# Kernel tuning notes

Hardware: AMD Instinct MI355X
Metric: run time of the kernel (lower is better)

The kernel has to match this reference:

```python
import jax, jax.numpy as jnp
import numpy as np

EPS = 1e-5
B, S, D = 4, 2048, 128
BALL_SCALE = 0.05  # keeps points inside the unit Poincare ball for c=1


def setup_inputs() -> dict:
    key = jax.random.key(0)
    kq, kk, kv = jax.random.split(key, 3)
    q = jax.random.normal(kq, (B, S, D), dtype=jnp.float32) * BALL_SCALE
    k = jax.random.normal(kk, (B, S, D), dtype=jnp.float32) * BALL_SCALE
    v_tangent = jax.random.normal(kv, (B, S, D), dtype=jnp.float32)
    c = jnp.asarray(1.0, dtype=jnp.float32)
    beta = jnp.asarray(0.0, dtype=jnp.float32)            # nn.Parameter init 0.0
    attention_bias = jnp.asarray(0.0, dtype=jnp.float32)  # nn.Parameter init 0.0
    return {"q": q, "k": k, "v_tangent": v_tangent, "c": c,
            "beta": beta, "attention_bias": attention_bias}


def reference(q, k, v_tangent, c, beta, attention_bias):
    sqrt_c = jnp.sqrt(c)

    # --- pairwise Poincare distance (all fp32, as in the torch autocast block) ---
    x_norm_sq = jnp.sum(q * q, axis=-1, keepdims=True)            # (B,S,1)
    y_norm_sq = jnp.sum(k * k, axis=-1, keepdims=True)            # (B,S,1)
    xy_dot = jnp.einsum('bsd,btd->bst', q, k)                     # (B,S,S)
    y_norm_sq_t = jnp.swapaxes(y_norm_sq, -2, -1)                 # (B,1,S)
    diff_norm_sq = x_norm_sq - 2.0 * xy_dot + y_norm_sq_t         # ||x-y||^2, (B,S,S)
    denom = (1.0 - c * x_norm_sq) * (1.0 - c * y_norm_sq_t)       # (B,S,S)
    arg = 1.0 + 2.0 * c * diff_norm_sq / jnp.maximum(denom, EPS)
    dist = jnp.arccosh(jnp.maximum(arg, 1.0 + EPS)) / sqrt_c      # (B,S,S)

    # --- attention ---
    beta_positive = jax.nn.softplus(beta)
    attention_scores = -beta_positive * dist - attention_bias
    attention_weights = jax.nn.softmax(attention_scores, axis=-1)  # (B,S,S)
    output_tangent = jnp.einsum('bst,btd->bsd', attention_weights, v_tangent)

    # --- exp map at origin ---
    v_norm = jnp.maximum(
        jnp.sqrt(jnp.sum(output_tangent * output_tangent, axis=-1, keepdims=True)), EPS)
    output_hyperbolic = (jnp.tanh(sqrt_c * v_norm) / sqrt_c) * (output_tangent / v_norm)

    return output_hyperbolic, attention_weights
```

## Files before the change

kernel.cpp:

```cpp
#include <hip/hip_runtime.h>
#include <math.h>

#define B_ 4
#define S_ 2048
#define D_ 128
#define EPSF 1e-5f
#define BN 128
#define PSB 272

typedef __attribute__((ext_vector_type(8))) short short8;
typedef __attribute__((ext_vector_type(4))) float f32x4;

static __device__ __forceinline__ unsigned short f2bf(float f) {
    unsigned u = __float_as_uint(f);
    return (unsigned short)((u + 0x7fffu + ((u >> 16) & 1u)) >> 16);
}

static __device__ __forceinline__ void gload_lds16(const void* g, void* l) {
    __builtin_amdgcn_global_load_lds((const __attribute__((address_space(1))) unsigned*)g,
                                     (__attribute__((address_space(3))) unsigned*)l, 16, 0, 0);
}


__global__ __launch_bounds__(256) void convqk_kernel(const float* __restrict__ q,
                                                     const float* __restrict__ k,
                                                     const float* __restrict__ cp,
                                                     float* __restrict__ qn, float* __restrict__ kn,
                                                     float* __restrict__ lws,
                                                     float2* __restrict__ qng, float2* __restrict__ kng,
                                                     unsigned* __restrict__ Qb, unsigned* __restrict__ Kb) {
    int row = blockIdx.x * 4 + (threadIdx.x >> 6);
    int lane = threadIdx.x & 63;
    const int NR = B_ * S_;
    const float cc = cp[0];
    bool isQ = row < NR;
    int r = isQ ? row : row - NR;
    float2 v = ((const float2*)(isQ ? q : k))[(size_t)r * 64 + lane];
    unsigned pk = (unsigned)f2bf(v.x) | ((unsigned)f2bf(v.y) << 16);
    float nrm = v.x * v.x + v.y * v.y;
#pragma unroll
    for (int m = 1; m <= 32; m <<= 1) nrm += __shfl_xor(nrm, m, 64);
    if (isQ) {
        Qb[(size_t)r * 64 + lane] = pk;
        if (lane == 0) {
            qn[r] = nrm;
            qng[r] = make_float2(nrm, 2.f * cc * __builtin_amdgcn_rcpf(1.f - cc * nrm));
        }
        if (lane == 1) lws[r] = 0.f;
    } else {
        int c = lane >> 2;
        int cs = c ^ (r & 7);
        Kb[(size_t)r * 64 + cs * 4 + (lane & 3)] = pk;
        if (lane == 0) {
            kn[r] = nrm;
            kng[r] = make_float2(nrm, __builtin_amdgcn_rcpf(1.f - cc * nrm));
        }
    }
}

__global__ __launch_bounds__(256) void convv_kernel(const float* __restrict__ v, uint4* __restrict__ Vtb) {
    __shared__ unsigned short Vs[128 * 132];
    int b = blockIdx.x >> 4;
    int t = blockIdx.x & 15;
    int tid = threadIdx.x;
    const float* src = v + ((size_t)b * S_ + t * 128) * D_;
    int d4 = tid & 31, key0 = tid >> 5;
#pragma unroll
    for (int it = 0; it < 16; ++it) {
        int key = key0 + it * 8;
        float4 f = *(const float4*)(src + (size_t)key * D_ + d4 * 4);
        unsigned short* dst = &Vs[key * 132 + d4 * 4];
        dst[0] = f2bf(f.x); dst[1] = f2bf(f.y); dst[2] = f2bf(f.z); dst[3] = f2bf(f.w);
    }
    __syncthreads();
    uint4* tile = Vtb + (size_t)blockIdx.x * (128 * 16);
    int d = tid & 127;
    int cl = tid >> 7;
#pragma unroll
    for (int it = 0; it < 8; ++it) {
        int c = cl + it * 2;
        int kb = c * 8;
        unsigned short e0 = Vs[(kb + 0) * 132 + d], e1 = Vs[(kb + 1) * 132 + d];
        unsigned short e2 = Vs[(kb + 2) * 132 + d], e3 = Vs[(kb + 3) * 132 + d];
        unsigned short e4 = Vs[(kb + 4) * 132 + d], e5 = Vs[(kb + 5) * 132 + d];
        unsigned short e6 = Vs[(kb + 6) * 132 + d], e7 = Vs[(kb + 7) * 132 + d];
        uint4 o;
        o.x = (unsigned)e0 | ((unsigned)e1 << 16);
        o.y = (unsigned)e2 | ((unsigned)e3 << 16);
        o.z = (unsigned)e4 | ((unsigned)e5 << 16);
        o.w = (unsigned)e6 | ((unsigned)e7 << 16);
        tile[d * 16 + (c ^ (d & 7))] = o;
    }
}


__global__ __launch_bounds__(1024, 4) void hattn5_kernel(
    const unsigned short* __restrict__ Qb, const char* __restrict__ Kb, const char* __restrict__ Vtb,
    const float2* __restrict__ qng, const float2* __restrict__ kng,
    const float* __restrict__ cp, const float* __restrict__ betap, const float* __restrict__ biasp,
    uint4* __restrict__ Pws, float* __restrict__ hout, float* __restrict__ wout) {

    __shared__ __align__(1024) char smem[142336];
    char* PsB = smem + 131072;
    float* l_row = (float*)(smem + 142080);
    float* nsq_s = (float*)(smem + 142208);

    const int tid = threadIdx.x;
    const int lane = tid & 63, wave = tid >> 6;
    const int wm = wave & 1, wn = wave >> 1;
    const int lm = lane & 15, quad = lane >> 4;

    int xcd = blockIdx.x & 7;
    int b = xcd >> 1;
    int rb = (blockIdx.x >> 3) * 2 + (xcd & 1);
    int s0 = rb * 32;
    const size_t bS = (size_t)b * S_;

    const float beta = betap[0], bias = biasp[0];
    const float cc = cp[0];
    const float beta_pos = fmaxf(beta, 0.f) + log1pf(__expf(-fabsf(beta)));
    const float sqrt_c = sqrtf(cc);
    const float bneg = -beta_pos / sqrt_c;
    const float bias2 = -bias * 1.442695040888963f;
    const float onepe = 1.f + EPSF;

    const char* KbBase = Kb + bS * 256;
    const char* VtBase = Vtb + (size_t)b * 16 * 32768;

    {
#pragma unroll
        for (int j = 0; j < 2; ++j) {
            int m = tid + j * 1024;
            gload_lds16(KbBase + m * 16, smem + m * 16);
            gload_lds16(VtBase + m * 16, smem + 65536 + m * 16);
        }
        if (tid < 128) {
            float2 y = kng[bS + tid];
            *(float2*)(smem + 139776 + tid * 8) = y;
        } else if (tid < 160) {
            float2 x = qng[bS + s0 + (tid - 128)];
            *(float2*)(smem + 141824 + (tid - 128) * 8) = x;
        } else if (tid < 192) {
            l_row[tid - 160] = 0.f;
        } else if (tid < 224) {
            nsq_s[tid - 192] = 0.f;
        }
    }

    short8 aq[4];
    {
        const unsigned short* qrow = Qb + (bS + s0 + wm * 16 + lm) * D_;
#pragma unroll
        for (int ks = 0; ks < 4; ++ks)
            aq[ks] = *(const short8*)(qrow + ks * 32 + quad * 8);
    }

    f32x4 o = {0.f, 0.f, 0.f, 0.f};
    float lacc[4] = {0.f, 0.f, 0.f, 0.f};

    __syncthreads();

    int p = 0;
    const int n0 = wn * 16 + lm;
    for (int it = 0; it < 16; ++it) {
        char* KsC = smem + p * 32768;
        char* VtC = smem + 65536 + p * 32768;
        const char* YGC = smem + 139776 + p * 1024;

        float2 ygn;
        if (it < 15) {
            const char* ks = KbBase + (size_t)(it + 1) * 32768;
            const char* vs = VtBase + (size_t)(it + 1) * 32768;
            char* kd = smem + (p ^ 1) * 32768;
            char* vd = smem + 65536 + (p ^ 1) * 32768;
#pragma unroll
            for (int j = 0; j < 2; ++j) {
                int off = (tid + j * 1024) * 16;
                gload_lds16(ks + off, kd + off);
                gload_lds16(vs + off, vd + off);
            }
            if (tid < 128) ygn = kng[bS + (size_t)(it + 1) * 128 + tid];
        }

        f32x4 acc = {0.f, 0.f, 0.f, 0.f};
#pragma unroll
        for (int ks = 0; ks < 4; ++ks) {
            int c = ks * 4 + quad;
            short8 bk = *(const short8*)(KsC + n0 * 256 + ((c ^ (n0 & 7)) * 16));
            acc = __builtin_amdgcn_mfma_f32_16x16x32_bf16(aq[ks], bk, acc, 0, 0, 0);
        }

        {
            float2 yg = *(const float2*)(YGC + n0 * 8);
#pragma unroll
            for (int r = 0; r < 4; ++r) {
                int row = wm * 16 + quad * 4 + r;
                float2 xr = *(const float2*)(smem + 141824 + row * 8);
                float diff = fmaf(-2.f, acc[r], xr.x + yg.x);
                float arg = fmaf(diff * yg.y, xr.y, 1.f);
                arg = fmaxf(arg, onepe);
                float w = arg + sqrtf(fmaf(arg, arg, -1.f));
                float pv = __builtin_amdgcn_exp2f(fmaf(bneg, __builtin_amdgcn_logf(w), bias2));
                *(unsigned short*)(PsB + row * PSB + n0 * 2) = f2bf(pv);
                lacc[r] += pv;
            }
        }
        __syncthreads();

        if (it < 15 && tid < 128) *(float2*)(smem + 139776 + (p ^ 1) * 1024 + tid * 8) = ygn;

        if (tid < 512) {
            int row = tid >> 4, ch = tid & 15;
            uint4 pv = *(const uint4*)(PsB + row * PSB + ch * 16);
            Pws[(((bS + s0 + row) * S_ + (size_t)it * 128) >> 3) + ch] = pv;
        }

#pragma unroll
        for (int ks = 0; ks < 4; ++ks) {
            short8 ap = *(const short8*)(PsB + (wm * 16 + lm) * PSB + (ks * 32 + quad * 8) * 2);
            int c = ks * 4 + quad;
            short8 vv = *(const short8*)(VtC + n0 * 256 + ((c ^ (n0 & 7)) * 16));
            o = __builtin_amdgcn_mfma_f32_16x16x32_bf16(ap, vv, o, 0, 0, 0);
        }
        __syncthreads();
        p ^= 1;
    }

#pragma unroll
    for (int r = 0; r < 4; ++r) {
        float s = lacc[r];
#pragma unroll
        for (int m = 1; m <= 8; m <<= 1) s += __shfl_xor(s, m, 64);
        if (lm == 0) atomicAdd(&l_row[wm * 16 + quad * 4 + r], s);
    }
    __syncthreads();

    float linv[4];
#pragma unroll
    for (int r = 0; r < 4; ++r) linv[r] = 1.f / l_row[wm * 16 + quad * 4 + r];

#pragma unroll
    for (int r = 0; r < 4; ++r) {
        float x = o[r] * linv[r];
        o[r] = x;
        float np = x * x;
#pragma unroll
        for (int m = 1; m <= 8; m <<= 1) np += __shfl_xor(np, m, 64);
        if (lm == 0) atomicAdd(&nsq_s[wm * 16 + quad * 4 + r], np);
    }
    __syncthreads();
#pragma unroll
    for (int r = 0; r < 4; ++r) {
        int row = wm * 16 + quad * 4 + r;
        float vn = fmaxf(sqrtf(nsq_s[row]), EPSF);
        float a = sqrt_c * vn;
        float th = 1.f - 2.f / (__expf(2.f * a) + 1.f);
        float sc = th / a;
        hout[(bS + s0 + row) * D_ + n0] = o[r] * sc;
    }

    {
        const uint4* psrc = Pws + (((bS + s0) * (size_t)S_) >> 3);
        float4* wdst = (float4*)(wout + (bS + s0) * (size_t)S_);
#pragma unroll
        for (int j = 0; j < 8; ++j) {
            int idx = tid + j * 1024;
            int row = idx >> 8;
            float lr = 1.f / l_row[row];
            uint4 u = psrc[idx];
            float4 f0, f1;
            f0.x = __uint_as_float(u.x << 16) * lr;
            f0.y = __uint_as_float(u.x & 0xffff0000u) * lr;
            f0.z = __uint_as_float(u.y << 16) * lr;
            f0.w = __uint_as_float(u.y & 0xffff0000u) * lr;
            f1.x = __uint_as_float(u.z << 16) * lr;
            f1.y = __uint_as_float(u.z & 0xffff0000u) * lr;
            f1.z = __uint_as_float(u.w << 16) * lr;
            f1.w = __uint_as_float(u.w & 0xffff0000u) * lr;
            wdst[idx * 2] = f0;
            wdst[idx * 2 + 1] = f1;
        }
    }
}


__global__ __launch_bounds__(512, 2) void hattn_kernel(
    const unsigned short* __restrict__ Qb, const char* __restrict__ Kb, const char* __restrict__ Vtb,
    const float* __restrict__ qn, const float* __restrict__ kn,
    const float* __restrict__ cp, const float* __restrict__ betap, const float* __restrict__ biasp,
    float* __restrict__ lws, float* __restrict__ houtg, float* __restrict__ woutg) {

    __shared__ __align__(1024) char smem[75136];
    char* KsB = smem;
    char* VtB = smem + 32768;
    char* PsB = smem + 65536;
    float* kn_s  = (float*)(smem + 74240);
    float* qn_s  = (float*)(smem + 74752);
    float* l_row = (float*)(smem + 74880);
    float* nsq_s = (float*)(smem + 75008);

    const int tid = threadIdx.x;
    const int lane = tid & 63, wave = tid >> 6;
    const int wm = wave & 1, wn = wave >> 1;
    const int lm = lane & 15, quad = lane >> 4;

    int xcd = blockIdx.x & 7;
    int b = xcd >> 1;
    int rb = (blockIdx.x >> 3) * 2 + (xcd & 1);
    int s0 = rb * 32;
    const size_t bS = (size_t)b * S_;

    const float cc = cp[0], beta = betap[0], bias = biasp[0];
    const float beta_pos = fmaxf(beta, 0.f) + log1pf(__expf(-fabsf(beta)));
    const float sqrt_c = sqrtf(cc);
    const float inv_sqrt_c = 1.f / sqrt_c;

    if (tid < 32) {
        qn_s[tid] = qn[bS + s0 + tid];
        l_row[tid] = 0.f;
        nsq_s[tid] = 0.f;
    }

    short8 aq[4];
    {
        const unsigned short* qrow = Qb + (bS + s0 + wm * 16 + lm) * D_;
#pragma unroll
        for (int ks = 0; ks < 4; ++ks)
            aq[ks] = *(const short8*)(qrow + ks * 32 + quad * 8);
    }

    f32x4 o0 = {0.f, 0.f, 0.f, 0.f}, o1 = {0.f, 0.f, 0.f, 0.f};

    const char* KbBase = Kb + bS * 256;
    const char* VtBase = Vtb + (size_t)b * 16 * 32768;

    for (int t = 0; t < S_ / BN; ++t) {
        int t0 = t * BN;
        __syncthreads();
        {
            const uint4* ksrc = (const uint4*)(KbBase + (size_t)t0 * 256);
            const uint4* vsrc = (const uint4*)(VtBase + (size_t)t * 32768);
            uint4* kd = (uint4*)KsB;
            uint4* vd = (uint4*)VtB;
#pragma unroll
            for (int i = 0; i < 4; ++i) {
                kd[tid + i * 512] = ksrc[tid + i * 512];
                vd[tid + i * 512] = vsrc[tid + i * 512];
            }
            if (tid < BN) kn_s[tid] = kn[bS + t0 + tid];
        }
        __syncthreads();

        f32x4 acc0 = {0.f, 0.f, 0.f, 0.f}, acc1 = {0.f, 0.f, 0.f, 0.f};
#pragma unroll
        for (int ks = 0; ks < 4; ++ks) {
            int n0 = wn * 32 + lm;
            int c = ks * 4 + quad;
            short8 b0 = *(const short8*)(KsB + n0 * 256 + ((c ^ (n0 & 7)) * 16));
            int n1 = n0 + 16;
            short8 b1 = *(const short8*)(KsB + n1 * 256 + ((c ^ (n1 & 7)) * 16));
            acc0 = __builtin_amdgcn_mfma_f32_16x16x32_bf16(aq[ks], b0, acc0, 0, 0, 0);
            acc1 = __builtin_amdgcn_mfma_f32_16x16x32_bf16(aq[ks], b1, acc1, 0, 0, 0);
        }

        float lp[4];
#pragma unroll
        for (int r = 0; r < 4; ++r) {
            int row = wm * 16 + quad * 4 + r;
            float xn = qn_s[row];
            float fx = 1.f - cc * xn;
            float p0, p1;
#pragma unroll
            for (int nt = 0; nt < 2; ++nt) {
                int col = wn * 32 + nt * 16 + lm;
                float dot = (nt == 0) ? acc0[r] : acc1[r];
                float yn = kn_s[col];
                float diff = xn - 2.f * dot + yn;
                float den = fmaxf(fx * (1.f - cc * yn), EPSF);
                float arg = fmaf(2.f * cc * diff, __builtin_amdgcn_rcpf(den), 1.f);
                arg = fmaxf(arg, 1.f + EPSF);
                float dist = __logf(arg + sqrtf(arg * arg - 1.f)) * inv_sqrt_c;
                float p = __expf(fmaf(-beta_pos, dist, -bias));
                woutg[(bS + s0 + row) * S_ + t0 + col] = p;
                *(unsigned short*)(PsB + row * PSB + col * 2) = f2bf(p);
                if (nt == 0) p0 = p; else p1 = p;
            }
            lp[r] = p0 + p1;
        }
#pragma unroll
        for (int r = 0; r < 4; ++r) {
            float s = lp[r];
#pragma unroll
            for (int m = 1; m <= 8; m <<= 1) s += __shfl_xor(s, m, 64);
            if (lm == 0) atomicAdd(&l_row[wm * 16 + quad * 4 + r], s);
        }
        __syncthreads();

#pragma unroll
        for (int ks = 0; ks < 4; ++ks) {
            short8 ap = *(const short8*)(PsB + (wm * 16 + lm) * PSB + (ks * 32 + quad * 8) * 2);
            int d0 = wn * 32 + lm;
            int c = ks * 4 + quad;
            short8 v0 = *(const short8*)(VtB + d0 * 256 + ((c ^ (d0 & 7)) * 16));
            int d1 = d0 + 16;
            short8 v1 = *(const short8*)(VtB + d1 * 256 + ((c ^ (d1 & 7)) * 16));
            o0 = __builtin_amdgcn_mfma_f32_16x16x32_bf16(ap, v0, o0, 0, 0, 0);
            o1 = __builtin_amdgcn_mfma_f32_16x16x32_bf16(ap, v1, o1, 0, 0, 0);
        }
    }
    __syncthreads();

    float xs0[4], xs1[4];
#pragma unroll
    for (int r = 0; r < 4; ++r) {
        int row = wm * 16 + quad * 4 + r;
        float linv = __builtin_amdgcn_rcpf(l_row[row]);
        float x0 = o0[r] * linv, x1 = o1[r] * linv;
        xs0[r] = x0; xs1[r] = x1;
        float np = x0 * x0 + x1 * x1;
#pragma unroll
        for (int m = 1; m <= 8; m <<= 1) np += __shfl_xor(np, m, 64);
        if (lm == 0) atomicAdd(&nsq_s[row], np);
    }
    if (tid < 32) lws[bS + s0 + tid] = l_row[tid];
    __syncthreads();
#pragma unroll
    for (int r = 0; r < 4; ++r) {
        int row = wm * 16 + quad * 4 + r;
        float vn = fmaxf(sqrtf(nsq_s[row]), EPSF);
        float a = sqrt_c * vn;
        float th = 1.f - 2.f * __builtin_amdgcn_rcpf(__expf(2.f * a) + 1.f);
        float sc = th / a;
        houtg[(bS + s0 + row) * D_ + wn * 32 + lm] = xs0[r] * sc;
        houtg[(bS + s0 + row) * D_ + wn * 32 + 16 + lm] = xs1[r] * sc;
    }
}

__global__ __launch_bounds__(256) void wnorm_kernel(float* __restrict__ w,
                                                    const float* __restrict__ lws) {
    size_t idx = (size_t)blockIdx.x * 256 + threadIdx.x;
    int row = (int)(idx >> 9);
    float linv = 1.f / lws[row];
    float4* p = (float4*)w + idx;
    float4 v = *p;
    v.x *= linv; v.y *= linv; v.z *= linv; v.w *= linv;
    *p = v;
}


extern "C" void kernel_launch(void* const* d_in, const int* in_sizes, int n_in,
                              void* d_out, int out_size, void* d_ws, size_t ws_size,
                              hipStream_t stream) {
    const float* q    = (const float*)d_in[0];
    const float* k    = (const float*)d_in[1];
    const float* v    = (const float*)d_in[2];
    const float* c    = (const float*)d_in[3];
    const float* beta = (const float*)d_in[4];
    const float* ab   = (const float*)d_in[5];

    float* out  = (float*)d_out;
    float* hout = out;
    float* wout = out + (size_t)B_ * S_ * D_;

    float* qn  = (float*)d_ws;
    float* kn  = qn + B_ * S_;
    float* lws = kn + B_ * S_;
    char*  wsb = (char*)d_ws;
    const size_t QG_OFF = 98304;
    const size_t KG_OFF = QG_OFF + 65536;
    const size_t QB_OFF = KG_OFF + 65536;
    const size_t KB_OFF = QB_OFF + 2097152;
    const size_t VT_OFF = KB_OFF + 2097152;
    const size_t NEED1  = VT_OFF + 2097152;
    const size_t PW_OFF = NEED1;
    const size_t NEED2  = PW_OFF + (size_t)B_ * S_ * S_ * 2;

    float2*  qng = (float2*)(wsb + QG_OFF);
    float2*  kng = (float2*)(wsb + KG_OFF);
    unsigned* Qb = (unsigned*)(wsb + QB_OFF);
    unsigned* Kb = (unsigned*)(wsb + KB_OFF);
    uint4*   Vtb = (uint4*)(wsb + VT_OFF);

    if (ws_size >= NEED2) {
        uint4* Pws = (uint4*)(wsb + PW_OFF);
        convqk_kernel<<<4096, 256, 0, stream>>>(q, k, c, qn, kn, lws, qng, kng, Qb, Kb);
        convv_kernel<<<64, 256, 0, stream>>>(v, Vtb);
        hattn5_kernel<<<256, 1024, 0, stream>>>((const unsigned short*)Qb, (const char*)Kb,
                                                (const char*)Vtb, qng, kng, c, beta, ab,
                                                Pws, hout, wout);
    } else {
        convqk_kernel<<<4096, 256, 0, stream>>>(q, k, c, qn, kn, lws, qng, kng, Qb, Kb);
        convv_kernel<<<64, 256, 0, stream>>>(v, Vtb);
        hattn_kernel<<<256, 512, 0, stream>>>((const unsigned short*)Qb, (const char*)Kb,
                                              (const char*)Vtb, qn, kn, c, beta, ab,
                                              lws, hout, wout);
        wnorm_kernel<<<(B_ * S_ * S_ / 4) / 256, 256, 0, stream>>>(wout, lws);
    }
}
```

Baseline: 147.6 us.

## Keep full probability row block in LDS and stream K/V fragments into registers

The attention kernel now keeps the whole 32x2048 bf16 probability block in shared memory instead of spilling each 128-column tile to a global workspace and reading it back for normalization. K and V tiles are no longer staged through LDS with async global-to-LDS copies. Each wave loads its own K and V fragments straight from global memory into registers, prefetching the next K tile one step ahead. This removes a global round trip of the probability matrix and one barrier per iteration, but it loses the shared LDS reuse of K/V across waves and exposes global load latency.

```diff
diff --git a/kernel.cpp b/kernel.cpp
--- a/kernel.cpp
+++ b/kernel.cpp
@@ -7,6 +7,7 @@
 #define EPSF 1e-5f
 #define BN 128
 #define PSB 272
+#define PRS 4112
 
 typedef __attribute__((ext_vector_type(8))) short short8;
 typedef __attribute__((ext_vector_type(4))) float f32x4;
@@ -14,11 +15,6 @@
 static __device__ __forceinline__ unsigned short f2bf(float f) {
     unsigned u = __float_as_uint(f);
     return (unsigned short)((u + 0x7fffu + ((u >> 16) & 1u)) >> 16);
-}
-
-static __device__ __forceinline__ void gload_lds16(const void* g, void* l) {
-    __builtin_amdgcn_global_load_lds((const __attribute__((address_space(1))) unsigned*)g,
-                                     (__attribute__((address_space(3))) unsigned*)l, 16, 0, 0);
 }
 
 
@@ -94,16 +90,15 @@
 }
 
 
-__global__ __launch_bounds__(1024, 4) void hattn5_kernel(
+__global__ __launch_bounds__(1024, 4) void hattn6_kernel(
     const unsigned short* __restrict__ Qb, const char* __restrict__ Kb, const char* __restrict__ Vtb,
     const float2* __restrict__ qng, const float2* __restrict__ kng,
     const float* __restrict__ cp, const float* __restrict__ betap, const float* __restrict__ biasp,
-    uint4* __restrict__ Pws, float* __restrict__ hout, float* __restrict__ wout) {
-
-    __shared__ __align__(1024) char smem[142336];
-    char* PsB = smem + 131072;
-    float* l_row = (float*)(smem + 142080);
-    float* nsq_s = (float*)(smem + 142208);
+    float* __restrict__ hout, float* __restrict__ wout) {
+
+    __shared__ __align__(1024) char smem[132096];
+    float* l_row = (float*)(smem + 131840);
+    float* nsq_s = (float*)(smem + 131968);
 
     const int tid = threadIdx.x;
     const int lane = tid & 63, wave = tid >> 6;
@@ -127,24 +122,26 @@
     const char* KbBase = Kb + bS * 256;
     const char* VtBase = Vtb + (size_t)b * 16 * 32768;
 
+    if (tid < 32) {
+        float2 x = qng[bS + s0 + tid];
+        *(float2*)(smem + 131584 + tid * 8) = x;
+    } else if (tid < 64) {
+        l_row[tid - 32] = 0.f;
+    } else if (tid < 96) {
+        nsq_s[tid - 64] = 0.f;
+    }
+
+    const int n0 = wn * 16 + lm;
+    short8 kf[4];
+    float2 yg;
     {
-#pragma unroll
-        for (int j = 0; j < 2; ++j) {
-            int m = tid + j * 1024;
-            gload_lds16(KbBase + m * 16, smem + m * 16);
-            gload_lds16(VtBase + m * 16, smem + 65536 + m * 16);
-        }
-        if (tid < 128) {
-            float2 y = kng[bS + tid];
-            *(float2*)(smem + 139776 + tid * 8) = y;
-        } else if (tid < 160) {
-            float2 x = qng[bS + s0 + (tid - 128)];
-            *(float2*)(smem + 141824 + (tid - 128) * 8) = x;
-        } else if (tid < 192) {
-            l_row[tid - 160] = 0.f;
-        } else if (tid < 224) {
-            nsq_s[tid - 192] = 0.f;
-        }
+        const char* kb0 = KbBase + n0 * 256;
+#pragma unroll
+        for (int ks = 0; ks < 4; ++ks) {
+            int c = ks * 4 + quad;
+            kf[ks] = *(const short8*)(kb0 + ((c ^ (n0 & 7)) * 16));
+        }
+        yg = kng[bS + n0];
     }
 
     short8 aq[4];
@@ -155,75 +152,71 @@
             aq[ks] = *(const short8*)(qrow + ks * 32 + quad * 8);
     }
 
+    __syncthreads();
+
+    float2 xr4[4];
+#pragma unroll
+    for (int r = 0; r < 4; ++r)
+        xr4[r] = *(const float2*)(smem + 131584 + (wm * 16 + quad * 4 + r) * 8);
+
     f32x4 o = {0.f, 0.f, 0.f, 0.f};
     float lacc[4] = {0.f, 0.f, 0.f, 0.f};
 
-    __syncthreads();
-
-    int p = 0;
-    const int n0 = wn * 16 + lm;
     for (int it = 0; it < 16; ++it) {
-        char* KsC = smem + p * 32768;
-        char* VtC = smem + 65536 + p * 32768;
-        const char* YGC = smem + 139776 + p * 1024;
-
+        f32x4 acc = {0.f, 0.f, 0.f, 0.f};
+#pragma unroll
+        for (int ks = 0; ks < 4; ++ks)
+            acc = __builtin_amdgcn_mfma_f32_16x16x32_bf16(aq[ks], kf[ks], acc, 0, 0, 0);
+
+        short8 kfn[4];
         float2 ygn;
         if (it < 15) {
-            const char* ks = KbBase + (size_t)(it + 1) * 32768;
-            const char* vs = VtBase + (size_t)(it + 1) * 32768;
-            char* kd = smem + (p ^ 1) * 32768;
-            char* vd = smem + 65536 + (p ^ 1) * 32768;
-#pragma unroll
-            for (int j = 0; j < 2; ++j) {
-                int off = (tid + j * 1024) * 16;
-                gload_lds16(ks + off, kd + off);
-                gload_lds16(vs + off, vd + off);
+            const char* kb = KbBase + (size_t)(it + 1) * 32768 + n0 * 256;
+#pragma unroll
+            for (int ks = 0; ks < 4; ++ks) {
+                int c = ks * 4 + quad;
+                kfn[ks] = *(const short8*)(kb + ((c ^ (n0 & 7)) * 16));
             }
-            if (tid < 128) ygn = kng[bS + (size_t)(it + 1) * 128 + tid];
-        }
-
-        f32x4 acc = {0.f, 0.f, 0.f, 0.f};
-#pragma unroll
-        for (int ks = 0; ks < 4; ++ks) {
-            int c = ks * 4 + quad;
-            short8 bk = *(const short8*)(KsC + n0 * 256 + ((c ^ (n0 & 7)) * 16));
-            acc = __builtin_amdgcn_mfma_f32_16x16x32_bf16(aq[ks], bk, acc, 0, 0, 0);
-        }
-
+            ygn = kng[bS + (size_t)(it + 1) * 128 + n0];
+        }
+
+        short8 vf[4];
         {
-            float2 yg = *(const float2*)(YGC + n0 * 8);
-#pragma unroll
-            for (int r = 0; r < 4; ++r) {
-                int row = wm * 16 + quad * 4 + r;
-                float2 xr = *(const float2*)(smem + 141824 + row * 8);
-                float diff = fmaf(-2.f, acc[r], xr.x + yg.x);
-                float arg = fmaf(diff * yg.y, xr.y, 1.f);
-                arg = fmaxf(arg, onepe);
-                float w = arg + sqrtf(fmaf(arg, arg, -1.f));
-                float pv = __builtin_amdgcn_exp2f(fmaf(bneg, __builtin_amdgcn_logf(w), bias2));
-                *(unsigned short*)(PsB + row * PSB + n0 * 2) = f2bf(pv);
-                lacc[r] += pv;
+            const char* vb = VtBase + (size_t)it * 32768 + n0 * 256;
+#pragma unroll
+            for (int ks = 0; ks < 4; ++ks) {
+                int c = ks * 4 + quad;
+                vf[ks] = *(const short8*)(vb + ((c ^ (n0 & 7)) * 16));
             }
         }
+
+#pragma unroll
+        for (int r = 0; r < 4; ++r) {
+            int row = wm * 16 + quad * 4 + r;
+            float diff = fmaf(-2.f, acc[r], xr4[r].x + yg.x);
+            float arg = fmaf(diff * yg.y, xr4[r].y, 1.f);
+            arg = fmaxf(arg, onepe);
+            float w = arg + sqrtf(fmaf(arg, arg, -1.f));
+            float pv = __builtin_amdgcn_exp2f(fmaf(bneg, __builtin_amdgcn_logf(w), bias2));
+            *(unsigned short*)(smem + row * PRS + (it * 128 + n0) * 2) = f2bf(pv);
+            lacc[r] += pv;
+        }
         __syncthreads();
 
-        if (it < 15 && tid < 128) *(float2*)(smem + 139776 + (p ^ 1) * 1024 + tid * 8) = ygn;
-
-        if (tid < 512) {
-            int row = tid >> 4, ch = tid & 15;
-            uint4 pv = *(const uint4*)(PsB + row * PSB + ch * 16);
-            Pws[(((bS + s0 + row) * S_ + (size_t)it * 128) >> 3) + ch] = pv;
-        }
-
-#pragma unroll
-        for (int ks = 0; ks < 4; ++ks) {
-            short8 ap = *(const short8*)(PsB + (wm * 16 + lm) * PSB + (ks * 32 + quad * 8) * 2);
-            int c = ks * 4 + quad;
-            short8 vv = *(const short8*)(VtC + n0 * 256 + ((c ^ (n0 & 7)) * 16));
-            o = __builtin_amdgcn_mfma_f32_16x16x32_bf16(ap, vv, o, 0, 0, 0);
-        }
-        __syncthreads();
-        p ^= 1;
+        {
+            const char* prow = smem + (wm * 16 + lm) * PRS + it * 256 + quad * 16;
+#pragma unroll
+            for (int ks = 0; ks < 4; ++ks) {
+                short8 ap = *(const short8*)(prow + ks * 64);
+                o = __builtin_amdgcn_mfma_f32_16x16x32_bf16(ap, vf[ks], o, 0, 0, 0);
+            }
+        }
+
+        if (it < 15) {
+#pragma unroll
+            for (int ks = 0; ks < 4; ++ks) kf[ks] = kfn[ks];
+            yg = ygn;
+        }
     }
 
 #pragma unroll
@@ -260,14 +253,14 @@
     }
 
     {
-        const uint4* psrc = Pws + (((bS + s0) * (size_t)S_) >> 3);
         float4* wdst = (float4*)(wout + (bS + s0) * (size_t)S_);
 #pragma unroll
         for (int j = 0; j < 8; ++j) {
             int idx = tid + j * 1024;
             int row = idx >> 8;
+            int ch = idx & 255;
             float lr = 1.f / l_row[row];
-            uint4 u = psrc[idx];
+            uint4 u = *(const uint4*)(smem + row * PRS + ch * 16);
             float4 f0, f1;
             f0.x = __uint_as_float(u.x << 16) * lr;
             f0.y = __uint_as_float(u.x & 0xffff0000u) * lr;
@@ -472,8 +465,6 @@
     const size_t KB_OFF = QB_OFF + 2097152;
     const size_t VT_OFF = KB_OFF + 2097152;
     const size_t NEED1  = VT_OFF + 2097152;
-    const size_t PW_OFF = NEED1;
-    const size_t NEED2  = PW_OFF + (size_t)B_ * S_ * S_ * 2;
 
     float2*  qng = (float2*)(wsb + QG_OFF);
     float2*  kng = (float2*)(wsb + KG_OFF);
@@ -481,13 +472,12 @@
     unsigned* Kb = (unsigned*)(wsb + KB_OFF);
     uint4*   Vtb = (uint4*)(wsb + VT_OFF);
 
-    if (ws_size >= NEED2) {
-        uint4* Pws = (uint4*)(wsb + PW_OFF);
+    if (ws_size >= NEED1) {
         convqk_kernel<<<4096, 256, 0, stream>>>(q, k, c, qn, kn, lws, qng, kng, Qb, Kb);
         convv_kernel<<<64, 256, 0, stream>>>(v, Vtb);
-        hattn5_kernel<<<256, 1024, 0, stream>>>((const unsigned short*)Qb, (const char*)Kb,
+        hattn6_kernel<<<256, 1024, 0, stream>>>((const unsigned short*)Qb, (const char*)Kb,
                                                 (const char*)Vtb, qng, kng, c, beta, ab,
-                                                Pws, hout, wout);
+                                                hout, wout);
     } else {
         convqk_kernel<<<4096, 256, 0, stream>>>(q, k, c, qn, kn, lws, qng, kng, Qb, Kb);
         convv_kernel<<<64, 256, 0, stream>>>(v, Vtb);
```

New measurement: 136.8 us (median of 2 runs). 1.08x faster.
